# Kernel tuning notes

Measured on AMD Instinct MI355X. Metric: run time of the kernel, lower is better.

Reference implementation:

```python
import jax, jax.numpy as jnp
import numpy as np

ALPHA = 0.2  # LeakyReLU negative slope
NEG = -9e15


def _gat_heads(x, adj_mask, W, a):
    # x: (B,N,F); W: (H,F,O); a: (H,2O); adj_mask: (B,N,N) bool
    O = W.shape[-1]
    Wh = jnp.einsum('bnf,hfo->bhno', x, W)            # (B,H,N,O)
    e1 = jnp.einsum('bhno,ho->bhn', Wh, a[:, :O])     # Wh @ a[:O]
    e2 = jnp.einsum('bhno,ho->bhn', Wh, a[:, O:])     # Wh @ a[O:]
    e = jax.nn.leaky_relu(e1[:, :, :, None] + e2[:, :, None, :], ALPHA)  # (B,H,N,N)
    e = jnp.where(adj_mask[:, None], e, NEG)
    attn = jax.nn.softmax(e, axis=-1)
    return jnp.einsum('bhnm,bhmo->bhno', attn, Wh)    # (B,H,N,O)


def _gat_block(x, adj_mask, non_pad_mask, W_heads, a_heads, W_out, a_out):
    # multi-head layer, concat=True -> elu per head, then concat on feature dim
    h = jax.nn.elu(_gat_heads(x, adj_mask, W_heads, a_heads))  # (B,H,N,O)
    B, H, N, O = h.shape
    h = jnp.transpose(h, (0, 2, 1, 3)).reshape(B, N, H * O)
    h = h * non_pad_mask
    # out layer: single head, concat=False (no inner elu)
    h = _gat_heads(h, adj_mask, W_out[None], a_out[None])[:, 0]  # (B,N,noutput)
    h = h * non_pad_mask
    return jax.nn.elu(h)


def setup_inputs() -> dict:
    key = jax.random.key(0)
    ks = jax.random.split(key, 8)
    B, N = 32, 256
    vocab, F, O, H, OUT = 200, 300, 256, 8, 512
    fea = jax.random.randint(ks[0], (B, N), 0, vocab, dtype=jnp.int32)
    adj = jax.random.randint(ks[1], (B, N, N), 0, 2, dtype=jnp.int32)
    non_pad_mask = jnp.ones((B, N, 1), dtype=jnp.float32)
    embed = jax.random.normal(ks[2], (vocab, F), dtype=jnp.float32)
    W_heads = jax.random.normal(ks[3], (H, F, O), dtype=jnp.float32) / np.sqrt(F)
    a_heads = jax.random.normal(ks[4], (H, 2 * O), dtype=jnp.float32) / np.sqrt(2 * O)
    W_out = jax.random.normal(ks[5], (H * O, OUT), dtype=jnp.float32) / np.sqrt(H * O)
    a_out = jax.random.normal(ks[6], (2 * OUT,), dtype=jnp.float32) / np.sqrt(2 * OUT)
    return {"fea": fea, "adj": adj, "non_pad_mask": non_pad_mask, "embed": embed,
            "W_heads": W_heads, "a_heads": a_heads, "W_out": W_out, "a_out": a_out}


def reference(fea, adj, non_pad_mask, embed, W_heads, a_heads, W_out, a_out):
    adj_mask = adj > 0
    x = embed[fea]  # (B,N,F)
    # GAT_num = 1; dropout is identity in eval mode
    x = _gat_block(x, adj_mask, non_pad_mask, W_heads, a_heads, W_out, a_out)
    return x  # (B, N, 512)
```

## Files before the change

kernel.cpp:

```cpp
#include <hip/hip_runtime.h>
#include <math.h>


typedef _Float16 f16;
typedef __attribute__((ext_vector_type(8))) _Float16 f16x8;
typedef __attribute__((ext_vector_type(4))) _Float16 f16x4;
typedef __attribute__((ext_vector_type(4))) float f32x4;
typedef unsigned long long u64;

__device__ __forceinline__ void async16(const void* g, void* lds) {
  __builtin_amdgcn_global_load_lds(
      (const __attribute__((address_space(1))) void*)g,
      (__attribute__((address_space(3))) void*)lds, 16, 0, 0);
}

__global__ __launch_bounds__(256) void k_prep(const int* __restrict__ fea,
                                              const float* __restrict__ embed,
                                              const float* __restrict__ Whd,
                                              const float* __restrict__ Wo,
                                              const int* __restrict__ adj,
                                              f16* __restrict__ x16,
                                              f16* __restrict__ WcT,
                                              f16* __restrict__ WoT,
                                              float* __restrict__ e_all,
                                              u64* __restrict__ adjG) {
  int bid = blockIdx.x, tid = threadIdx.x;
  if (bid < 1280) {
    int idx = bid * 256 + tid;
    int row = idx / 40, c = idx % 40;
    int tok = fea[row];
    const float* eb = embed + (size_t)tok * 300;
    f16x8 v;
    if (c < 37) {
      float4 f0 = *(const float4*)&eb[c * 8];
      float4 f1 = *(const float4*)&eb[c * 8 + 4];
      v[0] = (f16)f0.x; v[1] = (f16)f0.y; v[2] = (f16)f0.z; v[3] = (f16)f0.w;
      v[4] = (f16)f1.x; v[5] = (f16)f1.y; v[6] = (f16)f1.z; v[7] = (f16)f1.w;
    } else {
#pragma unroll
      for (int j = 0; j < 8; ++j) {
        int t = c * 8 + j;
        v[j] = (f16)((t < 300) ? eb[t] : 0.f);
      }
    }
    *(f16x8*)&x16[(size_t)row * 320 + c * 8] = v;
  } else if (bid < 1920) {
    int r = bid - 1280;
    int zi = r * 256 + tid;
    if (zi < 16384) e_all[zi] = 0.f;
    __shared__ float tile[32][33];
    int bx = r % 10, q0 = r / 10;
    int by = q0 % 8, h = q0 / 8;
    int c = tid & 31, q = tid >> 5;
#pragma unroll
    for (int i = 0; i < 4; ++i) {
      int tt = q + i * 8;
      int t = bx * 32 + tt;
      float v = (t < 300) ? Whd[((size_t)h * 300 + t) * 256 + by * 32 + c] : 0.f;
      tile[tt][c] = v;
    }
    __syncthreads();
#pragma unroll
    for (int i = 0; i < 4; ++i) {
      int oo = q + i * 8;
      int gc = h * 256 + by * 32 + oo;
      WcT[(size_t)gc * 320 + bx * 32 + c] = (f16)tile[c][oo];
    }
  } else if (bid < 2944) {
    int r = bid - 1920;
    __shared__ float tile[32][33];
    int bx = r % 64, by = r / 64;
    int c = tid & 31, q = tid >> 5;
#pragma unroll
    for (int i = 0; i < 4; ++i) {
      int kk = q + i * 8;
      tile[kk][c] = Wo[((size_t)bx * 32 + kk) * 512 + by * 32 + c];
    }
    __syncthreads();
#pragma unroll
    for (int i = 0; i < 4; ++i) {
      int oo = q + i * 8;
      WoT[((size_t)by * 32 + oo) * 2048 + bx * 32 + c] = (f16)tile[c][oo];
    }
  } else {
    int r = bid - 2944;
    int wv = tid >> 6, ln = tid & 63;
    int row = r * 64 + wv * 16;
    const int* ar = adj + (size_t)row * 256;
#pragma unroll 4
    for (int i = 0; i < 16; ++i, ar += 256) {
      u64 m0 = __ballot(ar[ln] != 0);
      u64 m1 = __ballot(ar[64 + ln] != 0);
      u64 m2 = __ballot(ar[128 + ln] != 0);
      u64 m3 = __ballot(ar[192 + ln] != 0);
      if (ln == 0) {
        u64* d = &adjG[(size_t)(row + i) * 4];
        d[0] = m0; d[1] = m1; d[2] = m2; d[3] = m3;
      }
    }
  }
}

__global__ __launch_bounds__(512, 1) void k_l1(
    const f16* __restrict__ x16, const f16* __restrict__ WcT,
    const float* __restrict__ ah, const u64* __restrict__ adjG,
    const float* __restrict__ npm, f16* __restrict__ h1) {
  extern __shared__ __align__(16) char smem[];
  f16* AsB[2] = {(f16*)smem, (f16*)(smem + 65536)};
  f16* BsB[2] = {(f16*)(smem + 32768), (f16*)(smem + 98304)};
  char* WhB = smem;
  u64* adjB = (u64*)(smem + 131072);
  float* e1f = (float*)(smem + 139264);
  float* e2f = (float*)(smem + 140288);

  const int bid = blockIdx.x;
  const int h = (bid >> 3) & 7;
  const int b = (bid & 7) * 4 + (bid >> 6);
  const int tid = threadIdx.x;
  const int wave = tid >> 6, lane = tid & 63;
  const int wm = wave >> 2, wn = wave & 3;
  const int lrow = lane & 15, quad = lane >> 4;
  const int srow = lane >> 3;
  const int scol = ((lane & 7) ^ (lane >> 3)) * 8;
  const int l7 = lrow & 7;

  if (tid < 256) e1f[tid] = 0.f;
  else e2f[tid - 256] = 0.f;

  f32x4 acc[8][4] = {};
  const f16* Ag = x16 + (size_t)b * 256 * 320;
  const f16* Bg = WcT + (size_t)h * 256 * 320;

  async16((const char*)adjG + (size_t)b * 8192 + tid * 16, (char*)adjB + tid * 16);
#pragma unroll
  for (int j = 0; j < 4; ++j) {
    const int r0 = wave * 32 + j * 8;
    async16(Ag + (size_t)(r0 + srow) * 320 + scol, &AsB[0][r0 * 64]);
    async16(Bg + (size_t)(r0 + srow) * 320 + scol, &BsB[0][r0 * 64]);
  }
  __syncthreads();

#pragma unroll
  for (int t = 0; t < 5; ++t) {
    const f16* As = AsB[t & 1];
    const f16* Bs = BsB[t & 1];
    if (t < 4) {
      const int kn = (t + 1) * 64;
      f16* An = AsB[(t + 1) & 1];
      f16* Bn = BsB[(t + 1) & 1];
#pragma unroll
      for (int j = 0; j < 4; ++j) {
        const int r0 = wave * 32 + j * 8;
        async16(Ag + (size_t)(r0 + srow) * 320 + kn + scol, &An[r0 * 64]);
        async16(Bg + (size_t)(r0 + srow) * 320 + kn + scol, &Bn[r0 * 64]);
      }
    }
#pragma unroll
    for (int s = 0; s < 2; ++s) {
      const int sq = ((s * 4 + quad) ^ l7) * 8;
      f16x8 af[8], bf[4];
#pragma unroll
      for (int mt = 0; mt < 8; ++mt)
        af[mt] = *(const f16x8*)&As[(wm * 128 + mt * 16 + lrow) * 64 + sq];
#pragma unroll
      for (int nt = 0; nt < 4; ++nt)
        bf[nt] = *(const f16x8*)&Bs[(wn * 64 + nt * 16 + lrow) * 64 + sq];
#pragma unroll
      for (int mt = 0; mt < 8; ++mt)
#pragma unroll
        for (int nt = 0; nt < 4; ++nt)
          acc[mt][nt] = __builtin_amdgcn_mfma_f32_16x16x32_f16(af[mt], bf[nt], acc[mt][nt], 0, 0, 0);
    }
    __syncthreads();
  }

  float a1v[4], a2v[4];
#pragma unroll
  for (int nt = 0; nt < 4; ++nt) {
    const int o = wn * 64 + nt * 16 + lrow;
    a1v[nt] = ah[h * 512 + o];
    a2v[nt] = ah[h * 512 + 256 + o];
  }
#pragma unroll
  for (int mt = 0; mt < 8; ++mt) {
    const int n0 = wm * 128 + mt * 16 + quad * 4;
    const int q16 = n0 >> 3;
    const int hoff = (n0 & 4) ? 8 : 0;
    float s1[4] = {0.f, 0.f, 0.f, 0.f}, s2[4] = {0.f, 0.f, 0.f, 0.f};
#pragma unroll
    for (int nt = 0; nt < 4; ++nt) {
      const int o = wn * 64 + nt * 16 + lrow;
      f16x4 v;
#pragma unroll
      for (int r = 0; r < 4; ++r) {
        v[r] = (f16)acc[mt][nt][r];
        s1[r] += acc[mt][nt][r] * a1v[nt];
        s2[r] += acc[mt][nt][r] * a2v[nt];
      }
      *(f16x4*)(WhB + o * 512 + ((q16 ^ (o & 7)) * 16 + hoff)) = v;
    }
#pragma unroll
    for (int r = 0; r < 4; ++r)
#pragma unroll
      for (int m = 1; m < 16; m <<= 1) {
        s1[r] += __shfl_xor(s1[r], m);
        s2[r] += __shfl_xor(s2[r], m);
      }
    if (lrow == 0) {
#pragma unroll
      for (int r = 0; r < 4; ++r) {
        atomicAdd(&e1f[n0 + r], s1[r]);
        atomicAdd(&e2f[n0 + r], s2[r]);
      }
    }
  }
  __syncthreads();

  float4 e2q = *(const float4*)&e2f[lane * 4];
  float e2m = fmaxf(fmaxf(e2q.x, e2q.y), fmaxf(e2q.z, e2q.w));
#pragma unroll
  for (int m = 1; m < 64; m <<= 1) e2m = fmaxf(e2m, __shfl_xor(e2m, m));

  const int nb0 = wave * 32;
  const float er0 = e1f[nb0 + lrow];
  const float er1 = e1f[nb0 + 16 + lrow];
  float sh0 = er0 + e2m; sh0 = sh0 > 0.f ? sh0 : 0.2f * sh0;
  float sh1 = er1 + e2m; sh1 = sh1 > 0.f ? sh1 : 0.2f * sh1;
  u64 aw0[4], aw1[4];
#pragma unroll
  for (int q = 0; q < 4; ++q) {
    aw0[q] = adjB[(nb0 + lrow) * 4 + q];
    aw1[q] = adjB[(nb0 + 16 + lrow) * 4 + q];
  }

  f16x8 p0[8], p1[8];
  float ss0 = 0.f, ss1 = 0.f;
#pragma unroll
  for (int k0 = 0; k0 < 8; ++k0) {
    const float* e2p = &e2f[k0 * 32 + quad * 8];
    float4 ea = *(const float4*)e2p;
    float4 eb = *(const float4*)(e2p + 4);
    unsigned int b0 = (unsigned int)(aw0[k0 >> 1] >> ((k0 & 1) * 32 + quad * 8)) & 0xFFu;
    unsigned int b1 = (unsigned int)(aw1[k0 >> 1] >> ((k0 & 1) * 32 + quad * 8)) & 0xFFu;
    float e2arr[8] = {ea.x, ea.y, ea.z, ea.w, eb.x, eb.y, eb.z, eb.w};
    f16x8 q0, q1;
#pragma unroll
    for (int j = 0; j < 8; ++j) {
      float v = er0 + e2arr[j]; v = v > 0.f ? v : 0.2f * v;
      float p = (b0 >> j) & 1 ? __expf(v - sh0) : 0.f;
      ss0 += p; q0[j] = (f16)p;
      v = er1 + e2arr[j]; v = v > 0.f ? v : 0.2f * v;
      p = (b1 >> j) & 1 ? __expf(v - sh1) : 0.f;
      ss1 += p; q1[j] = (f16)p;
    }
    p0[k0] = q0; p1[k0] = q1;
  }
  ss0 += __shfl_xor(ss0, 16); ss0 += __shfl_xor(ss0, 32);
  ss1 += __shfl_xor(ss1, 16); ss1 += __shfl_xor(ss1, 32);
  const float rs0 = 1.f / ss0, rs1 = 1.f / ss1;
  const float pm0 = npm[b * 256 + nb0 + lrow];
  const float pm1 = npm[b * 256 + nb0 + 16 + lrow];
  f16* h1b0 = &h1[(size_t)(b * 256 + nb0 + lrow) * 2048 + h * 256];
  f16* h1b1 = &h1[(size_t)(b * 256 + nb0 + 16 + lrow) * 2048 + h * 256];
  const char* wp = WhB + (size_t)lrow * 512;

#pragma unroll 4
  for (int of = 0; of < 16; ++of) {
    f32x4 c0 = {}, c1 = {};
    const char* wo = wp + of * 8192;
#pragma unroll
    for (int k0 = 0; k0 < 8; ++k0) {
      f16x8 af = *(const f16x8*)(wo + (((k0 * 4 + quad) ^ l7) * 16));
      c0 = __builtin_amdgcn_mfma_f32_16x16x32_f16(af, p0[k0], c0, 0, 0, 0);
      c1 = __builtin_amdgcn_mfma_f32_16x16x32_f16(af, p1[k0], c1, 0, 0, 0);
    }
    const int o0 = of * 16 + quad * 4;
    f16x4 s0, s1;
#pragma unroll
    for (int r = 0; r < 4; ++r) {
      float v = c0[r] * rs0;
      v = v > 0.f ? v : (__expf(v) - 1.f);
      s0[r] = (f16)(v * pm0);
      v = c1[r] * rs1;
      v = v > 0.f ? v : (__expf(v) - 1.f);
      s1[r] = (f16)(v * pm1);
    }
    *(f16x4*)(h1b0 + o0) = s0;
    *(f16x4*)(h1b1 + o0) = s1;
  }
}

__global__ __launch_bounds__(256, 4) void k_gemm_sk(const f16* __restrict__ A,
                                                    const f16* __restrict__ BT,
                                                    f16* __restrict__ outW,
                                                    const float* __restrict__ ao,
                                                    float* __restrict__ e12,
                                                    float* __restrict__ e22) {
  __shared__ f16 As[64 * 64];
  __shared__ f16 Bs[64 * 64];
  const int bid = blockIdx.x;
  const int xcd = bid & 7, j = bid >> 3;
  const int bx = j & 7;
  const int by = xcd * 16 + (j >> 3);
  const int tid = threadIdx.x;
  const int wave = tid >> 6, lane = tid & 63;
  const int wm = wave >> 1, wn = wave & 1;
  const int lrow = lane & 15, quad = lane >> 4;
  const int srow = lane >> 3;
  const int scol = ((lane & 7) ^ (lane >> 3)) * 8;
  const int l7 = lrow & 7;

  f32x4 acc[2][2] = {};
  const f16* Ag = A + (size_t)by * 64 * 2048;
  const f16* Bg = BT + (size_t)bx * 64 * 2048;

  for (int k0 = 0; k0 < 2048; k0 += 64) {
    __syncthreads();
#pragma unroll
    for (int j2 = 0; j2 < 2; ++j2) {
      const int r0 = wave * 16 + j2 * 8;
      async16(Ag + (size_t)(r0 + srow) * 2048 + k0 + scol, &As[r0 * 64]);
      async16(Bg + (size_t)(r0 + srow) * 2048 + k0 + scol, &Bs[r0 * 64]);
    }
    __syncthreads();
#pragma unroll
    for (int s = 0; s < 2; ++s) {
      const int sq = ((s * 4 + quad) ^ l7) * 8;
      f16x8 af[2], bf[2];
#pragma unroll
      for (int t = 0; t < 2; ++t)
        af[t] = *(const f16x8*)&As[(wm * 32 + t * 16 + lrow) * 64 + sq];
#pragma unroll
      for (int t = 0; t < 2; ++t)
        bf[t] = *(const f16x8*)&Bs[(wn * 32 + t * 16 + lrow) * 64 + sq];
#pragma unroll
      for (int mt = 0; mt < 2; ++mt)
#pragma unroll
        for (int nt = 0; nt < 2; ++nt)
          acc[mt][nt] = __builtin_amdgcn_mfma_f32_16x16x32_f16(af[mt], bf[nt], acc[mt][nt], 0, 0, 0);
    }
  }

  const int b = (by * 64) >> 8;
  const int nbase0 = (by * 64) & 255;
#pragma unroll
  for (int mt = 0; mt < 2; ++mt) {
    const int nb = nbase0 + wm * 32 + mt * 16 + quad * 4;
#pragma unroll
    for (int nt = 0; nt < 2; ++nt) {
      const int gc = bx * 64 + wn * 32 + nt * 16 + lrow;
      f16x4 v;
#pragma unroll
      for (int r = 0; r < 4; ++r) v[r] = (f16)acc[mt][nt][r];
      *(f16x4*)&outW[((size_t)b * 512 + gc) * 256 + nb] = v;
    }
  }

  float a1v[2], a2v[2];
#pragma unroll
  for (int nt = 0; nt < 2; ++nt) {
    const int gc = bx * 64 + wn * 32 + nt * 16 + lrow;
    a1v[nt] = ao[gc];
    a2v[nt] = ao[512 + gc];
  }
#pragma unroll
  for (int mt = 0; mt < 2; ++mt) {
    float s1[4] = {0.f, 0.f, 0.f, 0.f}, s2[4] = {0.f, 0.f, 0.f, 0.f};
#pragma unroll
    for (int nt = 0; nt < 2; ++nt)
#pragma unroll
      for (int r = 0; r < 4; ++r) {
        s1[r] += acc[mt][nt][r] * a1v[nt];
        s2[r] += acc[mt][nt][r] * a2v[nt];
      }
#pragma unroll
    for (int r = 0; r < 4; ++r)
#pragma unroll
      for (int m = 1; m < 16; m <<= 1) {
        s1[r] += __shfl_xor(s1[r], m);
        s2[r] += __shfl_xor(s2[r], m);
      }
    if (lrow == 0) {
      const int nb = nbase0 + wm * 32 + mt * 16 + quad * 4;
#pragma unroll
      for (int r = 0; r < 4; ++r) {
        atomicAdd(&e12[b * 256 + nb + r], s1[r]);
        atomicAdd(&e22[b * 256 + nb + r], s2[r]);
      }
    }
  }
}

#define PSTRIDE 264

__global__ __launch_bounds__(256, 4) void k_attn2(
    const f16* __restrict__ Wh2, const float* __restrict__ e1g, const float* __restrict__ e2g,
    const u64* __restrict__ adjG, const float* __restrict__ npm, float* __restrict__ out) {
  int bid = blockIdx.x;
  int nt0 = (bid >> 3) & 3;
  int pair = (bid >> 5) * 8 + (bid & 7);
  int oh = pair >> 5, b = pair & 31;
  int n0 = nt0 * 64;
  __shared__ f16 P[64 * PSTRIDE];
  int tid = threadIdx.x;
  int wave = tid >> 6, lane = tid & 63;
  int lrow = lane & 15, quad = lane >> 4;

  const f16* Ag = Wh2 + ((size_t)b * 512 + oh * 128) * 256;
  f16x8 afp[2];
#pragma unroll
  for (int mt = 0; mt < 2; ++mt) {
    size_t off = (size_t)(wave * 32 + mt * 16 + lrow) * 256 + quad * 8;
    afp[mt] = *(const f16x8*)&Ag[off];
  }

  float4 e2v = *(const float4*)&e2g[b * 256 + lane * 4];
  float e2m = fmaxf(fmaxf(e2v.x, e2v.y), fmaxf(e2v.z, e2v.w));
#pragma unroll
  for (int m = 1; m < 64; m <<= 1) e2m = fmaxf(e2m, __shfl_xor(e2m, m));
#pragma unroll 4
  for (int i = 0; i < 16; ++i) {
    int row = i * 4 + wave;
    int gn = b * 256 + n0 + row;
    float er = e1g[b * 256 + n0 + row];
    float sh = er + e2m;
    sh = sh > 0.f ? sh : 0.2f * sh;
    u64 word = adjG[(size_t)gn * 4 + (lane >> 4)];
    unsigned int bits = (unsigned int)(word >> ((lane & 15) * 4)) & 0xFu;
    float p0, p1, p2, p3;
    {
      float v = er + e2v.x; v = v > 0.f ? v : 0.2f * v;
      p0 = bits & 1 ? __expf(v - sh) : 0.f;
      v = er + e2v.y; v = v > 0.f ? v : 0.2f * v;
      p1 = bits & 2 ? __expf(v - sh) : 0.f;
      v = er + e2v.z; v = v > 0.f ? v : 0.2f * v;
      p2 = bits & 4 ? __expf(v - sh) : 0.f;
      v = er + e2v.w; v = v > 0.f ? v : 0.2f * v;
      p3 = bits & 8 ? __expf(v - sh) : 0.f;
    }
    float sm = p0 + p1 + p2 + p3;
#pragma unroll
    for (int m = 1; m < 64; m <<= 1) sm += __shfl_xor(sm, m);
    float rs = 1.f / sm;
    f16x4 pw;
    pw[0] = (f16)(p0 * rs); pw[1] = (f16)(p1 * rs);
    pw[2] = (f16)(p2 * rs); pw[3] = (f16)(p3 * rs);
    *(f16x4*)&P[row * PSTRIDE + lane * 4] = pw;
  }
  __syncthreads();

  f32x4 acc[2][4] = {};
#pragma unroll
  for (int kk = 0; kk < 8; ++kk) {
    const int k0 = kk * 32;
    f16x8 af[2], bf[4];
#pragma unroll
    for (int mt = 0; mt < 2; ++mt) {
      if (kk == 0) {
        af[mt] = afp[mt];
      } else {
        size_t off = (size_t)(wave * 32 + mt * 16 + lrow) * 256 + k0 + quad * 8;
        af[mt] = *(const f16x8*)&Ag[off];
      }
    }
#pragma unroll
    for (int nt = 0; nt < 4; ++nt)
      bf[nt] = *(const f16x8*)&P[(nt * 16 + lrow) * PSTRIDE + k0 + quad * 8];
#pragma unroll
    for (int mt = 0; mt < 2; ++mt)
#pragma unroll
      for (int nt = 0; nt < 4; ++nt)
        acc[mt][nt] = __builtin_amdgcn_mfma_f32_16x16x32_f16(af[mt], bf[nt], acc[mt][nt], 0, 0, 0);
  }
#pragma unroll
  for (int nt = 0; nt < 4; ++nt) {
    int nloc = nt * 16 + lrow;
    int gn = b * 256 + n0 + nloc;
    float pm = npm[gn];
#pragma unroll
    for (int mt = 0; mt < 2; ++mt) {
      int o0 = oh * 128 + wave * 32 + mt * 16 + quad * 4;
      float4 st;
      float v0 = acc[mt][nt][0] * pm;
      float v1 = acc[mt][nt][1] * pm;
      float v2 = acc[mt][nt][2] * pm;
      float v3 = acc[mt][nt][3] * pm;
      st.x = v0 > 0.f ? v0 : (__expf(v0) - 1.f);
      st.y = v1 > 0.f ? v1 : (__expf(v1) - 1.f);
      st.z = v2 > 0.f ? v2 : (__expf(v2) - 1.f);
      st.w = v3 > 0.f ? v3 : (__expf(v3) - 1.f);
      *(float4*)&out[(size_t)gn * 512 + o0] = st;
    }
  }
}

extern "C" void kernel_launch(void* const* d_in, const int* in_sizes, int n_in,
                              void* d_out, int out_size, void* d_ws, size_t ws_size,
                              hipStream_t stream) {
  (void)in_sizes; (void)n_in; (void)out_size; (void)ws_size;
  const int*   fea   = (const int*)d_in[0];
  const int*   adj   = (const int*)d_in[1];
  const float* npm   = (const float*)d_in[2];
  const float* embed = (const float*)d_in[3];
  const float* Whd   = (const float*)d_in[4];
  const float* ah    = (const float*)d_in[5];
  const float* Wo    = (const float*)d_in[6];
  const float* ao    = (const float*)d_in[7];
  float* out = (float*)d_out;

  char* ws = (char*)d_ws;
  f16* x16  = (f16*)ws;  ws += (size_t)8192 * 320 * 2;
  f16* WcT  = (f16*)ws;  ws += (size_t)2048 * 320 * 2;
  f16* WoT  = (f16*)ws;  ws += (size_t)512 * 2048 * 2;
  f16* h1   = (f16*)ws;  ws += (size_t)8192 * 2048 * 2;
  f16* Wh2  = (f16*)ws;  ws += (size_t)32 * 512 * 256 * 2;
  float* e12 = (float*)ws; ws += (size_t)8192 * 4;
  float* e22 = (float*)ws; ws += (size_t)8192 * 4;
  u64* adjG = (u64*)ws;  ws += (size_t)8192 * 4 * 8;

  k_prep<<<3072, 256, 0, stream>>>(fea, embed, Whd, Wo, adj, x16, WcT, WoT, e12, adjG);

  k_l1<<<256, 512, 141312, stream>>>(x16, WcT, ah, adjG, npm, h1);

  k_gemm_sk<<<1024, 256, 0, stream>>>(h1, WoT, Wh2, ao, e12, e22);
  k_attn2<<<512, 256, 0, stream>>>(Wh2, e12, e22, adjG, npm, out);
}
```

Before: 167.8 us.

## Precompute Wo·a_out vectors and fold second-layer attention logits into layer one

Uses associativity to compute the output-layer attention logits as h1·(W_out·a_out) instead of (h1·W_out)·a_out. The projected vectors are built by new blocks in the prep kernel and loaded into LDS in the layer-one kernel, which accumulates the logits during its epilogue and adds them with atomics. This removes the shuffle reductions and atomics from the second GEMM epilogue. In exchange it adds prep work, a little extra LDS, and logits taken from fp32 values before the fp16 rounding of h1, so rounding differs slightly from before.

```diff
diff --git a/kernel.cpp b/kernel.cpp
--- a/kernel.cpp
+++ b/kernel.cpp
@@ -19,11 +19,13 @@
                                               const float* __restrict__ Whd,
                                               const float* __restrict__ Wo,
                                               const int* __restrict__ adj,
+                                              const float* __restrict__ ao,
                                               f16* __restrict__ x16,
                                               f16* __restrict__ WcT,
                                               f16* __restrict__ WoT,
                                               float* __restrict__ e_all,
-                                              u64* __restrict__ adjG) {
+                                              u64* __restrict__ adjG,
+                                              float* __restrict__ wo12G) {
   int bid = blockIdx.x, tid = threadIdx.x;
   if (bid < 1280) {
     int idx = bid * 256 + tid;
@@ -82,7 +84,7 @@
       int oo = q + i * 8;
       WoT[((size_t)by * 32 + oo) * 2048 + bx * 32 + c] = (f16)tile[c][oo];
     }
-  } else {
+  } else if (bid < 3072) {
     int r = bid - 2944;
     int wv = tid >> 6, ln = tid & 63;
     int row = r * 64 + wv * 16;
@@ -98,13 +100,31 @@
         d[0] = m0; d[1] = m1; d[2] = m2; d[3] = m3;
       }
     }
+  } else {
+    int r = bid - 3072;
+    __shared__ float a1s[512], a2s[512];
+    a1s[tid] = ao[tid];       a1s[256 + tid] = ao[256 + tid];
+    a2s[tid] = ao[512 + tid]; a2s[256 + tid] = ao[768 + tid];
+    __syncthreads();
+    int k = r * 256 + tid;
+    const float* wr = Wo + (size_t)k * 512;
+    float s1 = 0.f, s2 = 0.f;
+#pragma unroll 4
+    for (int o = 0; o < 512; o += 4) {
+      float4 w4 = *(const float4*)&wr[o];
+      s1 += w4.x * a1s[o] + w4.y * a1s[o + 1] + w4.z * a1s[o + 2] + w4.w * a1s[o + 3];
+      s2 += w4.x * a2s[o] + w4.y * a2s[o + 1] + w4.z * a2s[o + 2] + w4.w * a2s[o + 3];
+    }
+    wo12G[k] = s1;
+    wo12G[2048 + k] = s2;
   }
 }
 
 __global__ __launch_bounds__(512, 1) void k_l1(
     const f16* __restrict__ x16, const f16* __restrict__ WcT,
     const float* __restrict__ ah, const u64* __restrict__ adjG,
-    const float* __restrict__ npm, f16* __restrict__ h1) {
+    const float* __restrict__ npm, const float* __restrict__ wo12G,
+    f16* __restrict__ h1, float* __restrict__ e12G, float* __restrict__ e22G) {
   extern __shared__ __align__(16) char smem[];
   f16* AsB[2] = {(f16*)smem, (f16*)(smem + 65536)};
   f16* BsB[2] = {(f16*)(smem + 32768), (f16*)(smem + 98304)};
@@ -112,6 +132,7 @@
   u64* adjB = (u64*)(smem + 131072);
   float* e1f = (float*)(smem + 139264);
   float* e2f = (float*)(smem + 140288);
+  float* wol = (float*)(smem + 141312);
 
   const int bid = blockIdx.x;
   const int h = (bid >> 3) & 7;
@@ -132,6 +153,11 @@
   const f16* Bg = WcT + (size_t)h * 256 * 320;
 
   async16((const char*)adjG + (size_t)b * 8192 + tid * 16, (char*)adjB + tid * 16);
+  if (tid < 64)
+    async16((const char*)wo12G + (size_t)h * 1024 + tid * 16, (char*)wol + tid * 16);
+  else if (tid < 128)
+    async16((const char*)wo12G + 8192 + (size_t)h * 1024 + (tid - 64) * 16,
+            (char*)wol + 1024 + (tid - 64) * 16);
 #pragma unroll
   for (int j = 0; j < 4; ++j) {
     const int r0 = wave * 32 + j * 8;
@@ -264,6 +290,7 @@
   f16* h1b1 = &h1[(size_t)(b * 256 + nb0 + 16 + lrow) * 2048 + h * 256];
   const char* wp = WhB + (size_t)lrow * 512;
 
+  float e12p0 = 0.f, e22p0 = 0.f, e12p1 = 0.f, e22p1 = 0.f;
 #pragma unroll 4
   for (int of = 0; of < 16; ++of) {
     f32x4 c0 = {}, c1 = {};
@@ -278,24 +305,37 @@
     f16x4 s0, s1;
 #pragma unroll
     for (int r = 0; r < 4; ++r) {
+      float w1 = wol[o0 + r], w2 = wol[256 + o0 + r];
       float v = c0[r] * rs0;
       v = v > 0.f ? v : (__expf(v) - 1.f);
-      s0[r] = (f16)(v * pm0);
+      float hv0 = v * pm0;
+      s0[r] = (f16)hv0;
+      e12p0 += hv0 * w1; e22p0 += hv0 * w2;
       v = c1[r] * rs1;
       v = v > 0.f ? v : (__expf(v) - 1.f);
-      s1[r] = (f16)(v * pm1);
+      float hv1 = v * pm1;
+      s1[r] = (f16)hv1;
+      e12p1 += hv1 * w1; e22p1 += hv1 * w2;
     }
     *(f16x4*)(h1b0 + o0) = s0;
     *(f16x4*)(h1b1 + o0) = s1;
   }
+
+  e12p0 += __shfl_xor(e12p0, 16); e12p0 += __shfl_xor(e12p0, 32);
+  e22p0 += __shfl_xor(e22p0, 16); e22p0 += __shfl_xor(e22p0, 32);
+  e12p1 += __shfl_xor(e12p1, 16); e12p1 += __shfl_xor(e12p1, 32);
+  e22p1 += __shfl_xor(e22p1, 16); e22p1 += __shfl_xor(e22p1, 32);
+  if (lane < 16) {
+    atomicAdd(&e12G[b * 256 + nb0 + lrow], e12p0);
+    atomicAdd(&e22G[b * 256 + nb0 + lrow], e22p0);
+    atomicAdd(&e12G[b * 256 + nb0 + 16 + lrow], e12p1);
+    atomicAdd(&e22G[b * 256 + nb0 + 16 + lrow], e22p1);
+  }
 }
 
 __global__ __launch_bounds__(256, 4) void k_gemm_sk(const f16* __restrict__ A,
                                                     const f16* __restrict__ BT,
-                                                    f16* __restrict__ outW,
-                                                    const float* __restrict__ ao,
-                                                    float* __restrict__ e12,
-                                                    float* __restrict__ e22) {
+                                                    f16* __restrict__ outW) {
   __shared__ f16 As[64 * 64];
   __shared__ f16 Bs[64 * 64];
   const int bid = blockIdx.x;
@@ -353,40 +393,6 @@
 #pragma unroll
       for (int r = 0; r < 4; ++r) v[r] = (f16)acc[mt][nt][r];
       *(f16x4*)&outW[((size_t)b * 512 + gc) * 256 + nb] = v;
-    }
-  }
-
-  float a1v[2], a2v[2];
-#pragma unroll
-  for (int nt = 0; nt < 2; ++nt) {
-    const int gc = bx * 64 + wn * 32 + nt * 16 + lrow;
-    a1v[nt] = ao[gc];
-    a2v[nt] = ao[512 + gc];
-  }
-#pragma unroll
-  for (int mt = 0; mt < 2; ++mt) {
-    float s1[4] = {0.f, 0.f, 0.f, 0.f}, s2[4] = {0.f, 0.f, 0.f, 0.f};
-#pragma unroll
-    for (int nt = 0; nt < 2; ++nt)
-#pragma unroll
-      for (int r = 0; r < 4; ++r) {
-        s1[r] += acc[mt][nt][r] * a1v[nt];
-        s2[r] += acc[mt][nt][r] * a2v[nt];
-      }
-#pragma unroll
-    for (int r = 0; r < 4; ++r)
-#pragma unroll
-      for (int m = 1; m < 16; m <<= 1) {
-        s1[r] += __shfl_xor(s1[r], m);
-        s2[r] += __shfl_xor(s2[r], m);
-      }
-    if (lrow == 0) {
-      const int nb = nbase0 + wm * 32 + mt * 16 + quad * 4;
-#pragma unroll
-      for (int r = 0; r < 4; ++r) {
-        atomicAdd(&e12[b * 256 + nb + r], s1[r]);
-        atomicAdd(&e22[b * 256 + nb + r], s2[r]);
-      }
     }
   }
 }
@@ -517,11 +523,12 @@
   float* e12 = (float*)ws; ws += (size_t)8192 * 4;
   float* e22 = (float*)ws; ws += (size_t)8192 * 4;
   u64* adjG = (u64*)ws;  ws += (size_t)8192 * 4 * 8;
-
-  k_prep<<<3072, 256, 0, stream>>>(fea, embed, Whd, Wo, adj, x16, WcT, WoT, e12, adjG);
-
-  k_l1<<<256, 512, 141312, stream>>>(x16, WcT, ah, adjG, npm, h1);
-
-  k_gemm_sk<<<1024, 256, 0, stream>>>(h1, WoT, Wh2, ao, e12, e22);
+  float* wo12G = (float*)ws; ws += (size_t)2 * 2048 * 4;
+
+  k_prep<<<3080, 256, 0, stream>>>(fea, embed, Whd, Wo, adj, ao, x16, WcT, WoT, e12, adjG, wo12G);
+
+  k_l1<<<256, 512, 143360, stream>>>(x16, WcT, ah, adjG, npm, wo12G, h1, e12, e22);
+
+  k_gemm_sk<<<1024, 256, 0, stream>>>(h1, WoT, Wh2);
   k_attn2<<<512, 256, 0, stream>>>(Wh2, e12, e22, adjG, npm, out);
 }
```

After: 172.4 us. 1.03x slower.
